# Performance work log

Measured on AMD Instinct MI355X. Metric: run time of the kernel, lower is better.

Reference implementation:

```python
import jax, jax.numpy as jnp
import numpy as np

POOL = 7          # output pooling resolution (Mask R-CNN box head)
IMG = 1024.0      # assumed input image size (boxes are normalized)
CANON = 224.0     # canonical ROI size for FPN level assignment


def _make_boxes(key, B, N):
    k1, k2, k3, k4 = jax.random.split(key, 4)
    y1 = jax.random.uniform(k1, (B, N)) * 0.7
    x1 = jax.random.uniform(k2, (B, N)) * 0.7
    h = jax.random.uniform(k3, (B, N)) * 0.28 + 0.01
    w = jax.random.uniform(k4, (B, N)) * 0.28 + 0.01
    return jnp.stack([y1, x1, jnp.minimum(y1 + h, 1.0), jnp.minimum(x1 + w, 1.0)], axis=-1)


def setup_inputs() -> dict:
    key = jax.random.key(0)
    k3, k4, k5, k6, kb = jax.random.split(key, 5)
    B, C, N = 2, 256, 1000
    return {
        "p3": jax.random.normal(k3, (B, 128, 128, C), jnp.float32),
        "p4": jax.random.normal(k4, (B, 64, 64, C), jnp.float32),
        "p5": jax.random.normal(k5, (B, 32, 32, C), jnp.float32),
        "p6": jax.random.normal(k6, (B, 16, 16, C), jnp.float32),
        "proposals": _make_boxes(kb, B, N),
    }


def _crop_resize(f, boxes):
    # f: [H, W, C]; boxes: [N, 4] normalized (y1, x1, y2, x2).
    # Matches tf.image.crop_and_resize bilinear sampling (crop_size > 1).
    H, W, _ = f.shape
    y1, x1, y2, x2 = boxes[:, 0], boxes[:, 1], boxes[:, 2], boxes[:, 3]
    t = jnp.arange(POOL, dtype=f.dtype) / (POOL - 1)          # [P]
    ys = (y1[:, None] + t[None, :] * (y2 - y1)[:, None]) * (H - 1)  # [N, P]
    xs = (x1[:, None] + t[None, :] * (x2 - x1)[:, None]) * (W - 1)  # [N, P]
    y0f = jnp.floor(ys); x0f = jnp.floor(xs)
    fy = ys - y0f; fx = xs - x0f                                # fractional parts
    y0 = jnp.clip(y0f.astype(jnp.int32), 0, H - 1)
    y1i = jnp.clip(y0 + 1, 0, H - 1)
    x0 = jnp.clip(x0f.astype(jnp.int32), 0, W - 1)
    x1i = jnp.clip(x0 + 1, 0, W - 1)
    # gather 4 corners: index broadcast [N,P,1] x [N,1,P] -> [N,P,P,C]
    v00 = f[y0[:, :, None], x0[:, None, :]]
    v01 = f[y0[:, :, None], x1i[:, None, :]]
    v10 = f[y1i[:, :, None], x0[:, None, :]]
    v11 = f[y1i[:, :, None], x1i[:, None, :]]
    wy = fy[:, :, None, None]; wx = fx[:, None, :, None]
    top = v00 + wx * (v01 - v00)
    bot = v10 + wx * (v11 - v10)
    return top + wy * (bot - top)                               # [N, P, P, C]


def reference(p3, p4, p5, p6, proposals):
    # proposals: [B, N, 4] normalized (y1, x1, y2, x2)
    h = proposals[..., 2] - proposals[..., 0]
    w = proposals[..., 3] - proposals[..., 1]
    # FPN level assignment (levels 3..6)
    roi_level = jnp.log2(jnp.sqrt(jnp.maximum(h * w, 0.0)) / (CANON / IMG) + 1e-8)
    lvl = jnp.clip(4 + jnp.round(roi_level).astype(jnp.int32), 3, 6)  # [B, N]
    B, N = lvl.shape
    C = p3.shape[-1]
    pooled = jnp.zeros((B, N, POOL, POOL, C), p3.dtype)
    for li, f in zip((3, 4, 5, 6), (p3, p4, p5, p6)):
        p = jax.vmap(_crop_resize)(f, proposals)                # [B, N, P, P, C]
        pooled = jnp.where((lvl == li)[:, :, None, None, None], p, pooled)
    return pooled
```

## Files before the change

kernel.cpp:

```cpp
#include <hip/hip_runtime.h>

#define POOL 7
#define NPTS 49

typedef float f4 __attribute__((ext_vector_type(4)));

__device__ __forceinline__ f4 ld4(const float* p) { return *(const f4*)p; }

__device__ __forceinline__ int roi_level(float dy, float dx) {
    const float rl = log2f(sqrtf(fmaxf(dy * dx, 0.0f)) / 0.21875f + 1e-8f);
    int lvl = 4 + (int)rintf(rl);
    return lvl < 3 ? 3 : (lvl > 6 ? 6 : lvl);
}

__device__ __forceinline__ int bucket_key(const float* props, int r, int N) {
    const f4 p = ld4(props + (size_t)r * 4);
    const int lvl = roi_level(p.z - p.x, p.w - p.y);
    const float yc = 0.5f * (p.x + p.z);
    int oct = (int)(yc * 8.0f);
    oct = oct < 0 ? 0 : (oct > 7 ? 7 : oct);
    int lg = lvl - 3; lg = lg < 0 ? 0 : (lg > 1 ? 1 : lg);
    const int b = r >= N ? 1 : 0;
    return ((b << 1) | lg) * 8 + oct;
}

__global__ __launch_bounds__(1024) void bucket_kernel(
    const float* __restrict__ props, int* __restrict__ order, int BN, int N)
{
    __shared__ int hist[32];
    __shared__ int offs[32];
    const int tid = threadIdx.x;
    if (tid < 32) hist[tid] = 0;
    __syncthreads();
    for (int r = tid; r < BN; r += 1024)
        atomicAdd(&hist[bucket_key(props, r, N)], 1);
    __syncthreads();
    if (tid == 0) {
        int acc = 0;
        for (int i = 0; i < 32; ++i) { offs[i] = acc; acc += hist[i]; }
    }
    __syncthreads();
    for (int r = tid; r < BN; r += 1024) {
        const int k = bucket_key(props, r, N);
        const int pos = atomicAdd(&offs[k], 1);
        order[pos] = r;
    }
}

__global__ __launch_bounds__(256) void roialign_kernel(
    const float* __restrict__ p3, const float* __restrict__ p4,
    const float* __restrict__ p5, const float* __restrict__ p6,
    const float* __restrict__ props, const int* __restrict__ order,
    float* __restrict__ out, int B, int N, int C, int nwg)
{
    const int s   = blockIdx.x;
    const int q   = nwg >> 3, rr = nwg & 7;
    const int xcd = s & 7, idx = s >> 3;
    const int s2  = (xcd < rr ? xcd * (q + 1) : rr * (q + 1) + (xcd - rr) * q) + idx;
    const int roi = order[s2];
    const int b   = roi >= N ? 1 : 0;

    const f4 pv = ld4(props + (size_t)roi * 4);
    const float y1 = pv.x, x1 = pv.y, y2 = pv.z, x2 = pv.w;
    const float dy = y2 - y1, dx = x2 - x1;

    const int lvl = roi_level(dy, dx);
    const float* f;
    int H;
    if      (lvl == 3) { f = p3; H = 128; }
    else if (lvl == 4) { f = p4; H = 64;  }
    else if (lvl == 5) { f = p5; H = 32;  }
    else               { f = p6; H = 16;  }
    const int W = H;
    const float hm1 = (float)(H - 1);
    const float* fb = f + (size_t)b * H * W * C;

    const int tid = threadIdx.x;
    const int pl  = tid >> 6;
    const int cg  = (tid & 63) << 2;

    const int obase = roi * NPTS * C + cg;

    auto calc = [&](int p, int& o00, int& o01, int& o10, int& o11,
                    float& fx, float& fy) {
        const int py = p / POOL;
        const int px = p - py * POOL;
        const float ys = (y1 + (float)py * (1.0f / (POOL - 1)) * dy) * hm1;
        const float xs = (x1 + (float)px * (1.0f / (POOL - 1)) * dx) * hm1;
        const float y0f = floorf(ys);
        const float x0f = floorf(xs);
        fy = ys - y0f;
        fx = xs - x0f;
        int yA = (int)y0f; yA = yA < 0 ? 0 : (yA > H - 1 ? H - 1 : yA);
        int yB = yA + 1;   yB = yB > H - 1 ? H - 1 : yB;
        int xA = (int)x0f; xA = xA < 0 ? 0 : (xA > W - 1 ? W - 1 : xA);
        int xB = xA + 1;   xB = xB > W - 1 ? W - 1 : xB;
        const int rA = yA * W, rB = yB * W;
        o00 = (rA + xA) * C + cg;
        o01 = (rA + xB) * C + cg;
        o10 = (rB + xA) * C + cg;
        o11 = (rB + xB) * C + cg;
    };

    f4 oa_p, ob_p;
    int pa_p = -1, pb_p = -1;

    #pragma unroll
    for (int p0 = 0; p0 < 48; p0 += 8) {
        const int pa = p0 + pl;
        const int pb = pa + 4;
        int a00, a01, a10, a11, b00, b01, b10, b11;
        float afx, afy, bfx, bfy;
        calc(pa, a00, a01, a10, a11, afx, afy);
        calc(pb, b00, b01, b10, b11, bfx, bfy);

        const f4 va00 = ld4(fb + a00), va01 = ld4(fb + a01);
        const f4 va10 = ld4(fb + a10), va11 = ld4(fb + a11);
        const f4 vb00 = ld4(fb + b00), vb01 = ld4(fb + b01);
        const f4 vb10 = ld4(fb + b10), vb11 = ld4(fb + b11);

        if (pa_p >= 0) {
            __builtin_nontemporal_store(oa_p, (f4*)(out + obase + pa_p * C));
            __builtin_nontemporal_store(ob_p, (f4*)(out + obase + pb_p * C));
        }

        const f4 ta = va00 + afx * (va01 - va00);
        const f4 ba = va10 + afx * (va11 - va10);
        const f4 oa = ta + afy * (ba - ta);
        const f4 tb = vb00 + bfx * (vb01 - vb00);
        const f4 bb = vb10 + bfx * (vb11 - vb10);
        const f4 ob = tb + bfy * (bb - tb);

        oa_p = oa; ob_p = ob; pa_p = pa; pb_p = pb;
    }

    if (pl == 0) {
        int o00, o01, o10, o11;
        float fx, fy;
        calc(48, o00, o01, o10, o11, fx, fy);
        const f4 v00 = ld4(fb + o00), v01 = ld4(fb + o01);
        const f4 v10 = ld4(fb + o10), v11 = ld4(fb + o11);

        __builtin_nontemporal_store(oa_p, (f4*)(out + obase + pa_p * C));
        __builtin_nontemporal_store(ob_p, (f4*)(out + obase + pb_p * C));

        const f4 t  = v00 + fx * (v01 - v00);
        const f4 bo = v10 + fx * (v11 - v10);
        const f4 o  = t + fy * (bo - t);
        __builtin_nontemporal_store(o, (f4*)(out + obase + 48 * C));
    } else {
        __builtin_nontemporal_store(oa_p, (f4*)(out + obase + pa_p * C));
        __builtin_nontemporal_store(ob_p, (f4*)(out + obase + pb_p * C));
    }
}

extern "C" void kernel_launch(void* const* d_in, const int* in_sizes, int n_in,
                              void* d_out, int out_size, void* d_ws, size_t ws_size,
                              hipStream_t stream) {
    (void)ws_size; (void)n_in; (void)out_size;

    const float* p3 = (const float*)d_in[0];
    const float* p4 = (const float*)d_in[1];
    const float* p5 = (const float*)d_in[2];
    const float* p6 = (const float*)d_in[3];
    const float* props = (const float*)d_in[4];
    float* out = (float*)d_out;
    int* order = (int*)d_ws;

    const int B = 2;
    const int N = in_sizes[4] / (B * 4);
    const int C = in_sizes[0] / (B * 128 * 128);
    const int BN = B * N;

    bucket_kernel<<<1, 1024, 0, stream>>>(props, order, BN, N);
    roialign_kernel<<<BN, 256, 0, stream>>>(p3, p4, p5, p6, props, order,
                                            out, B, N, C, BN);
}
```

Before: 32.84 us.

## Balance per-XCD ROI schedule across level groups in bucketing kernel

The bucketing kernel now caches each ROI's key in shared memory. It builds a block-to-ROI schedule that splits every (batch, level-group) group evenly across the 8 XCDs, so each XCD's L2 sees a balanced share of every feature-map region. Overflow entries fill holes in under-filled XCD slots. This replaces the contiguous-chunk mapping that could leave some XCDs with uneven or mixed workloads. The scheduler does more serial and indexed logic on a single block, and keys are stored in a fixed 2048-byte array, which assumes BN <= 2048.

```diff
diff --git a/kernel.cpp b/kernel.cpp
--- a/kernel.cpp
+++ b/kernel.cpp
@@ -13,51 +13,96 @@
     return lvl < 3 ? 3 : (lvl > 6 ? 6 : lvl);
 }
 
-__device__ __forceinline__ int bucket_key(const float* props, int r, int N) {
-    const f4 p = ld4(props + (size_t)r * 4);
-    const int lvl = roi_level(p.z - p.x, p.w - p.y);
-    const float yc = 0.5f * (p.x + p.z);
-    int oct = (int)(yc * 8.0f);
-    oct = oct < 0 ? 0 : (oct > 7 ? 7 : oct);
-    int lg = lvl - 3; lg = lg < 0 ? 0 : (lg > 1 ? 1 : lg);
-    const int b = r >= N ? 1 : 0;
-    return ((b << 1) | lg) * 8 + oct;
-}
-
-__global__ __launch_bounds__(1024) void bucket_kernel(
-    const float* __restrict__ props, int* __restrict__ order, int BN, int N)
+__global__ __launch_bounds__(1024) void sched_kernel(
+    const float* __restrict__ props, int* __restrict__ sched, int BN, int N)
 {
+    __shared__ unsigned char keys[2048];
     __shared__ int hist[32];
-    __shared__ int offs[32];
+    __shared__ int bbase[32];
+    __shared__ int G[5];
+    __shared__ int q_[4], r_[4];
+    __shared__ int cnt[8];
+    __shared__ int goff[4][8];
+    __shared__ int cumHole[9], cumExtra[9];
+
     const int tid = threadIdx.x;
     if (tid < 32) hist[tid] = 0;
     __syncthreads();
-    for (int r = tid; r < BN; r += 1024)
-        atomicAdd(&hist[bucket_key(props, r, N)], 1);
+
+    for (int r = tid; r < BN; r += 1024) {
+        const f4 p = ld4(props + (size_t)r * 4);
+        const int lvl = roi_level(p.z - p.x, p.w - p.y);
+        int lg = lvl - 3; lg = lg < 0 ? 0 : (lg > 1 ? 1 : lg);
+        const float yc = 0.5f * (p.x + p.z);
+        int oct = (int)(yc * 8.0f);
+        oct = oct < 0 ? 0 : (oct > 7 ? 7 : oct);
+        const int bb = r >= N ? 1 : 0;
+        const int k = ((bb << 1) | lg) * 8 + oct;
+        keys[r] = (unsigned char)k;
+        atomicAdd(&hist[k], 1);
+    }
     __syncthreads();
+
     if (tid == 0) {
         int acc = 0;
-        for (int i = 0; i < 32; ++i) { offs[i] = acc; acc += hist[i]; }
+        for (int i = 0; i < 32; ++i) { bbase[i] = acc; acc += hist[i]; }
+        for (int g = 0; g < 4; ++g) G[g] = bbase[g * 8];
+        G[4] = BN;
+        for (int g = 0; g < 4; ++g) {
+            const int Sg = G[g + 1] - G[g];
+            q_[g] = Sg >> 3; r_[g] = Sg & 7;
+        }
+        for (int k = 0; k < 8; ++k) {
+            int a2 = 0;
+            for (int g = 0; g < 4; ++g) {
+                goff[g][k] = a2;
+                a2 += q_[g] + (k < r_[g] ? 1 : 0);
+            }
+            cnt[k] = a2;
+        }
+        const int nslot = BN >> 3;
+        int ch = 0, ce = 0;
+        for (int k = 0; k < 8; ++k) {
+            cumHole[k] = ch; cumExtra[k] = ce;
+            ch += cnt[k] < nslot ? nslot - cnt[k] : 0;
+            ce += cnt[k] > nslot ? cnt[k] - nslot : 0;
+        }
+        cumHole[8] = ch; cumExtra[8] = ce;
     }
     __syncthreads();
+
+    const int nslot = BN >> 3;
     for (int r = tid; r < BN; r += 1024) {
-        const int k = bucket_key(props, r, N);
-        const int pos = atomicAdd(&offs[k], 1);
-        order[pos] = r;
+        const int k = keys[r];
+        const int g = k >> 3;
+        const int p_old = atomicAdd(&bbase[k], 1);
+        const int rg = p_old - G[g];
+        const int qg = q_[g], rr = r_[g];
+        int sec, j;
+        if (rg < rr * (qg + 1)) { sec = rg / (qg + 1); j = rg - sec * (qg + 1); }
+        else { const int t = rg - rr * (qg + 1); sec = rr + t / qg; j = t - (sec - rr) * qg; }
+        const int o = goff[g][sec] + j;
+        int bid;
+        if (o < nslot) {
+            bid = o * 8 + sec;
+        } else {
+            const int e = cumExtra[sec] + (o - nslot);
+            int hk = 0;
+            while (!(e >= cumHole[hk] && e < cumHole[hk + 1])) ++hk;
+            const int ho = cnt[hk] + (e - cumHole[hk]);
+            bid = ho * 8 + hk;
+        }
+        sched[bid] = r;
     }
 }
 
 __global__ __launch_bounds__(256) void roialign_kernel(
     const float* __restrict__ p3, const float* __restrict__ p4,
     const float* __restrict__ p5, const float* __restrict__ p6,
-    const float* __restrict__ props, const int* __restrict__ order,
-    float* __restrict__ out, int B, int N, int C, int nwg)
+    const float* __restrict__ props, const int* __restrict__ sched,
+    float* __restrict__ out, int B, int N, int C)
 {
-    const int s   = blockIdx.x;
-    const int q   = nwg >> 3, rr = nwg & 7;
-    const int xcd = s & 7, idx = s >> 3;
-    const int s2  = (xcd < rr ? xcd * (q + 1) : rr * (q + 1) + (xcd - rr) * q) + idx;
-    const int roi = order[s2];
+    const int roi = sched[blockIdx.x];
     const int b   = roi >= N ? 1 : 0;
 
     const f4 pv = ld4(props + (size_t)roi * 4);
@@ -165,14 +210,14 @@
     const float* p6 = (const float*)d_in[3];
     const float* props = (const float*)d_in[4];
     float* out = (float*)d_out;
-    int* order = (int*)d_ws;
+    int* sched = (int*)d_ws;
 
     const int B = 2;
     const int N = in_sizes[4] / (B * 4);
     const int C = in_sizes[0] / (B * 128 * 128);
     const int BN = B * N;
 
-    bucket_kernel<<<1, 1024, 0, stream>>>(props, order, BN, N);
-    roialign_kernel<<<BN, 256, 0, stream>>>(p3, p4, p5, p6, props, order,
-                                            out, B, N, C, BN);
-}
+    sched_kernel<<<1, 1024, 0, stream>>>(props, sched, BN, N);
+    roialign_kernel<<<BN, 256, 0, stream>>>(p3, p4, p5, p6, props, sched,
+                                            out, B, N, C);
+}
```

Result: slower. 39.51 us (+20.3%).
